# Optimization experiments

Hardware: AMD Instinct MI355X
Metric: run time of the kernel (lower is better)

## Reference

```python
import jax, jax.numpy as jnp
import numpy as np

B, S, D = 16, 1024, 1024  # shape constraints force S == D == 1024


def setup_inputs() -> dict:
    key = jax.random.key(0)
    k1, k2, k3 = jax.random.split(key, 3)
    f1_norm = jax.random.normal(k1, (B, S, D), dtype=jnp.float32)
    f2_norm = jax.random.normal(k2, (B, S, D), dtype=jnp.float32)
    # xavier_normal_ init: std = sqrt(2 / (fan_in + fan_out))
    xavier_std = float(np.sqrt(2.0 / (D + D)))
    corr_weights = jax.random.normal(k3, (D, D), dtype=jnp.float32) * xavier_std
    return {"f1_norm": f1_norm, "f2_norm": f2_norm, "corr_weights": corr_weights}


def reference(f1_norm, f2_norm, corr_weights):
    # a1 = f1 @ W : [B, S, D]
    a1 = jnp.einsum('bsd,de->bse', f1_norm, corr_weights)
    # cc_mat = a1 @ f2^T : [B, S1, S2]
    cc_mat = jnp.einsum('bse,bte->bst', a1, f2_norm)
    audio_att = jax.nn.softmax(cc_mat, axis=1)                      # softmax over S1
    visual_att = jax.nn.softmax(jnp.swapaxes(cc_mat, 1, 2), axis=1)  # [B,S2,S1], softmax over S2
    atten_audiofeatures = jnp.matmul(f1_norm, audio_att)             # [B, S1(=D), S2]
    atten_visualfeatures = jnp.matmul(f2_norm, visual_att)           # [B, S2(=D), S1]
    return (jnp.swapaxes(atten_audiofeatures, 1, 2),
            jnp.swapaxes(atten_visualfeatures, 1, 2))
```

## Files before the change

### kernel.cpp

```cpp
#include <hip/hip_runtime.h>
#include <hip/hip_bf16.h>
#include <stdint.h>

typedef __bf16 bf16_t;
typedef bf16_t bf16x8 __attribute__((ext_vector_type(8)));
typedef bf16_t bf16x4 __attribute__((ext_vector_type(4)));
typedef float  f32x4  __attribute__((ext_vector_type(4)));

#define B_  16
#define S_  1024
#define D_  1024
#define BS_ (B_ * S_)
#define MAT_ (S_ * D_)

#define BAR()   __builtin_amdgcn_s_barrier()
#define LGKM0() asm volatile("s_waitcnt lgkmcnt(0)" ::: "memory")
#define VMC4()  asm volatile("s_waitcnt vmcnt(4)" ::: "memory")

__device__ __forceinline__ void async_load16(const void* g, void* l) {
    __builtin_amdgcn_global_load_lds((__attribute__((address_space(1))) void*)(g),
                                     (__attribute__((address_space(3))) void*)(l),
                                     16, 0, 0);
}

template <int SPLIT, int OSP, int XS, int STATS>
__global__ __launch_bounds__(512, 2)
void gemm8p(const bf16_t* __restrict__ gAh, const bf16_t* __restrict__ gAl,
            const bf16_t* __restrict__ gBh, const bf16_t* __restrict__ gBl,
            float* __restrict__ Cf, bf16_t* __restrict__ Ch, bf16_t* __restrict__ Cl,
            float* __restrict__ Mp2, float* __restrict__ Zp2,
            float* __restrict__ Np2, float* __restrict__ Yp2,
            int M, int N, int K, long sA, long sB, long sC)
{
    (void)M;
    constexpr int BK  = SPLIT ? 32 : 64;
    constexpr int BUF = 65536;
    __shared__ __attribute__((aligned(16))) char smem[2 * BUF];

    const int tid  = threadIdx.x;
    const int w    = tid >> 6;
    const int lane = tid & 63;
    const int wm   = w >> 2;
    const int wn   = w & 3;
    const int fm   = lane & 15;
    const int quad = lane >> 4;

    int bm, bn, b;
    if constexpr (XS == 1) {
        const int flat = (int)blockIdx.x + ((int)blockIdx.y << 2) + ((int)blockIdx.z << 4);
        const int xcd = flat & 7, slot = flat >> 3;
        b  = (xcd << 1) | (slot >> 4);
        bm = (slot >> 2) & 3;
        bn = slot & 3;
    } else if constexpr (XS == 2) {
        const int flat = (int)blockIdx.x + ((int)blockIdx.y << 2) + ((int)blockIdx.z << 4);
        const int xcd = flat & 7, slot = flat >> 3;
        b  = (xcd << 2) | (slot >> 4);
        bm = (slot >> 2) & 3;
        bn = slot & 3;
    } else if constexpr (XS == 3) {
        const int flat = (int)blockIdx.x + ((int)blockIdx.y << 2);
        const int xcd = flat & 7, slot = flat >> 3;
        b  = 0;
        bm = (xcd << 3) | (slot >> 2);
        bn = slot & 3;
    } else {
        bn = blockIdx.x; bm = blockIdx.y; b = blockIdx.z;
    }

    const bf16_t* pAh = gAh; const bf16_t* pAl = gAl;
    const bf16_t* pBh = gBh; const bf16_t* pBl = gBl;
    float* Cfp = Cf;
    if constexpr (XS == 2) {
        if (b >= 16) { pAh = gAl; pBh = gBl; Cfp = Cf + (long)B_ * MAT_; b -= 16; }
    }

    const int NT    = K / BK;
    const int abase = (int)((long)b * sA) + bm * 256 * K;
    const int bbase = (int)((long)b * sB) + bn * 256 * K;

    int aof[2][2], bof[2][2], lof[2][2];
    if constexpr (!SPLIT) {
#pragma unroll
        for (int h = 0; h < 2; ++h)
#pragma unroll
            for (int i = 0; i < 2; ++i) {
                const int o   = h * 16384 + i * 8192 + tid * 16;
                const int row = o >> 7;
                const int c   = ((o >> 4) & 7) ^ (row & 7);
                aof[h][i] = abase + row * K + c * 8;
                bof[h][i] = bbase + row * K + c * 8;
                lof[h][i] = o;
            }
    } else {
#pragma unroll
        for (int h = 0; h < 2; ++h) {
            const int o   = h * 8192 + tid * 16;
            const int row = o >> 6;
            const int c   = ((o >> 4) & 3) ^ ((row >> 1) & 3);
            aof[h][0] = abase + row * K + c * 8;
            bof[h][0] = bbase + row * K + c * 8;
            lof[h][0] = o;
        }
    }

    f32x4 acc[8][4] = {};

    if constexpr (!SPLIT) {
        auto stgA = [&](int t, int h, int lb) {
            const int k = (t < NT ? t : NT - 1) * BK;
            async_load16(pAh + (aof[h][0] + k), smem + lb + lof[h][0]);
            async_load16(pAh + (aof[h][1] + k), smem + lb + lof[h][1]);
        };
        auto stgB = [&](int t, int h, int lb) {
            const int k = (t < NT ? t : NT - 1) * BK;
            async_load16(pBh + (bof[h][0] + k), smem + lb + 32768 + lof[h][0]);
            async_load16(pBh + (bof[h][1] + k), smem + lb + 32768 + lof[h][1]);
        };
        const int xb = (fm & 7) << 4;
        auto ldA = [&](int lb, int m, int ks) -> bf16x8 {
            const int row = wm * 128 + m * 16 + fm;
            return *(const bf16x8*)(smem + lb + row * 128 + ((ks * 64 + quad * 16) ^ xb));
        };
        auto ldB = [&](int lb, int n, int ks) -> bf16x8 {
            const int row = wn * 64 + n * 16 + fm;
            return *(const bf16x8*)(smem + lb + 32768 + row * 128 + ((ks * 64 + quad * 16) ^ xb));
        };

        bf16x8 ar[4][2], br[4][2];
        auto qp = [&](int mh, int nh) {
#pragma unroll
            for (int m = 0; m < 4; ++m)
#pragma unroll
                for (int n = 0; n < 2; ++n) {
                    f32x4 c = acc[mh * 4 + m][nh * 2 + n];
                    c = __builtin_amdgcn_mfma_f32_16x16x32_bf16(ar[m][0], br[nh * 2 + n][0], c, 0, 0, 0);
                    c = __builtin_amdgcn_mfma_f32_16x16x32_bf16(ar[m][1], br[nh * 2 + n][1], c, 0, 0, 0);
                    acc[mh * 4 + m][nh * 2 + n] = c;
                }
        };

        stgA(0, 0, 0); stgA(0, 1, 0); stgB(0, 0, 0); stgB(0, 1, 0);
        stgB(1, 0, BUF); stgB(1, 1, BUF);
        VMC4(); BAR();

        const int NIT = NT >> 1;
        for (int it = 0; it < NIT; ++it) {
            const int t = it << 1;
#pragma unroll
            for (int ph = 0; ph < 2; ++ph) {
                const int rb = ph ? BUF : 0;
                const int ob = ph ? 0 : BUF;
                const int tt = t + ph;
#pragma unroll
                for (int m = 0; m < 4; ++m) { ar[m][0] = ldA(rb, m, 0); ar[m][1] = ldA(rb, m, 1); }
#pragma unroll
                for (int n = 0; n < 2; ++n) { br[n][0] = ldB(rb, n, 0); br[n][1] = ldB(rb, n, 1); }
                stgA(tt + 1, 0, ob);
                BAR(); LGKM0(); __builtin_amdgcn_s_setprio(1);
                qp(0, 0);
                __builtin_amdgcn_s_setprio(0); BAR();
#pragma unroll
                for (int n = 2; n < 4; ++n) { br[n][0] = ldB(rb, n, 0); br[n][1] = ldB(rb, n, 1); }
                stgA(tt + 1, 1, ob);
                BAR(); LGKM0(); __builtin_amdgcn_s_setprio(1);
                qp(0, 1);
                __builtin_amdgcn_s_setprio(0); BAR();
#pragma unroll
                for (int m = 0; m < 4; ++m) { ar[m][0] = ldA(rb, m + 4, 0); ar[m][1] = ldA(rb, m + 4, 1); }
                stgB(tt + 2, 0, rb);
                BAR(); LGKM0(); __builtin_amdgcn_s_setprio(1);
                qp(1, 0);
                __builtin_amdgcn_s_setprio(0); BAR();
                stgB(tt + 2, 1, rb);
                BAR(); LGKM0(); __builtin_amdgcn_s_setprio(1);
                qp(1, 1);
                __builtin_amdgcn_s_setprio(0); VMC4(); BAR();
            }
        }
    } else {
        auto stgAh = [&](int t, int lb) {
            const int k = (t < NT ? t : NT - 1) * BK;
            async_load16(pAh + (aof[0][0] + k), smem + lb + lof[0][0]);
            async_load16(pAh + (aof[1][0] + k), smem + lb + lof[1][0]);
        };
        auto stgAl = [&](int t, int lb) {
            const int k = (t < NT ? t : NT - 1) * BK;
            async_load16(pAl + (aof[0][0] + k), smem + lb + 16384 + lof[0][0]);
            async_load16(pAl + (aof[1][0] + k), smem + lb + 16384 + lof[1][0]);
        };
        auto stgBh = [&](int t, int lb) {
            const int k = (t < NT ? t : NT - 1) * BK;
            async_load16(pBh + (bof[0][0] + k), smem + lb + 32768 + lof[0][0]);
            async_load16(pBh + (bof[1][0] + k), smem + lb + 32768 + lof[1][0]);
        };
        auto stgBl = [&](int t, int lb) {
            const int k = (t < NT ? t : NT - 1) * BK;
            async_load16(pBl + (bof[0][0] + k), smem + lb + 49152 + lof[0][0]);
            async_load16(pBl + (bof[1][0] + k), smem + lb + 49152 + lof[1][0]);
        };
        const int xs2 = ((fm >> 1) & 3) << 4;
        auto ldSA = [&](int lb, int comp, int m) -> bf16x8 {
            const int row = wm * 128 + m * 16 + fm;
            return *(const bf16x8*)(smem + lb + comp * 16384 + row * 64 + ((quad * 16) ^ xs2));
        };
        auto ldSB = [&](int lb, int comp, int n) -> bf16x8 {
            const int row = wn * 64 + n * 16 + fm;
            return *(const bf16x8*)(smem + lb + comp * 16384 + row * 64 + ((quad * 16) ^ xs2));
        };

        bf16x8 arh[4], arl[4], brh[4], brl[4];
        auto qs = [&](int mh, int nh) {
#pragma unroll
            for (int m = 0; m < 4; ++m)
#pragma unroll
                for (int n = 0; n < 2; ++n) {
                    f32x4 c = acc[mh * 4 + m][nh * 2 + n];
                    c = __builtin_amdgcn_mfma_f32_16x16x32_bf16(arh[m], brh[nh * 2 + n], c, 0, 0, 0);
                    c = __builtin_amdgcn_mfma_f32_16x16x32_bf16(arl[m], brh[nh * 2 + n], c, 0, 0, 0);
                    c = __builtin_amdgcn_mfma_f32_16x16x32_bf16(arh[m], brl[nh * 2 + n], c, 0, 0, 0);
                    acc[mh * 4 + m][nh * 2 + n] = c;
                }
        };

        stgAh(0, 0); stgAl(0, 0); stgBh(0, 0); stgBl(0, 0);
        stgBh(1, BUF); stgBl(1, BUF);
        VMC4(); BAR();

        const int NIT = NT >> 1;
        for (int it = 0; it < NIT; ++it) {
            const int t = it << 1;
#pragma unroll
            for (int ph = 0; ph < 2; ++ph) {
                const int rb = ph ? BUF : 0;
                const int ob = ph ? 0 : BUF;
                const int tt = t + ph;
#pragma unroll
                for (int m = 0; m < 4; ++m) { arh[m] = ldSA(rb, 0, m); arl[m] = ldSA(rb, 1, m); }
#pragma unroll
                for (int n = 0; n < 2; ++n) { brh[n] = ldSB(rb, 2, n); brl[n] = ldSB(rb, 3, n); }
                stgAh(tt + 1, ob);
                BAR(); LGKM0(); __builtin_amdgcn_s_setprio(1);
                qs(0, 0);
                __builtin_amdgcn_s_setprio(0); BAR();
#pragma unroll
                for (int n = 2; n < 4; ++n) { brh[n] = ldSB(rb, 2, n); brl[n] = ldSB(rb, 3, n); }
                stgAl(tt + 1, ob);
                BAR(); LGKM0(); __builtin_amdgcn_s_setprio(1);
                qs(0, 1);
                __builtin_amdgcn_s_setprio(0); BAR();
#pragma unroll
                for (int m = 0; m < 4; ++m) { arh[m] = ldSA(rb, 0, m + 4); arl[m] = ldSA(rb, 1, m + 4); }
                stgBh(tt + 2, rb);
                BAR(); LGKM0(); __builtin_amdgcn_s_setprio(1);
                qs(1, 0);
                __builtin_amdgcn_s_setprio(0); BAR();
                stgBl(tt + 2, rb);
                BAR(); LGKM0(); __builtin_amdgcn_s_setprio(1);
                qs(1, 1);
                __builtin_amdgcn_s_setprio(0); VMC4(); BAR();
            }
        }
    }

    float2* colp = (float2*)smem;
    float2* rowp = (float2*)(smem + 4096);
    if constexpr (STATS) {
#pragma unroll
        for (int j = 0; j < 4; ++j) {
            float m = acc[0][j][0];
#pragma unroll
            for (int i = 0; i < 8; ++i)
#pragma unroll
                for (int r = 0; r < 4; ++r) m = fmaxf(m, acc[i][j][r]);
            float z = 0.f;
#pragma unroll
            for (int i = 0; i < 8; ++i)
#pragma unroll
                for (int r = 0; r < 4; ++r) z += __expf(acc[i][j][r] - m);
#pragma unroll
            for (int off = 16; off <= 32; off <<= 1) {
                float mo = __shfl_xor(m, off), zo = __shfl_xor(z, off);
                float nm = fmaxf(m, mo);
                z = z * __expf(m - nm) + zo * __expf(mo - nm); m = nm;
            }
            if (quad == 0) colp[wm * 256 + wn * 64 + j * 16 + fm] = make_float2(m, z);
        }
#pragma unroll
        for (int i = 0; i < 8; ++i)
#pragma unroll
            for (int r = 0; r < 4; ++r) {
                float m = fmaxf(fmaxf(acc[i][0][r], acc[i][1][r]),
                                fmaxf(acc[i][2][r], acc[i][3][r]));
                float z = __expf(acc[i][0][r] - m) + __expf(acc[i][1][r] - m)
                        + __expf(acc[i][2][r] - m) + __expf(acc[i][3][r] - m);
#pragma unroll
                for (int off = 1; off <= 8; off <<= 1) {
                    float mo = __shfl_xor(m, off), zo = __shfl_xor(z, off);
                    float nm = fmaxf(m, mo);
                    z = z * __expf(m - nm) + zo * __expf(mo - nm); m = nm;
                }
                if (fm == 0)
                    rowp[wn * 256 + wm * 128 + i * 16 + quad * 4 + r] = make_float2(m, z);
            }
    }

#pragma unroll
    for (int i = 0; i < 8; ++i) {
        const int row0 = bm * 256 + wm * 128 + i * 16 + quad * 4;
#pragma unroll
        for (int j = 0; j < 4; ++j) {
            const int col = bn * 256 + wn * 64 + j * 16 + fm;
#pragma unroll
            for (int r = 0; r < 4; ++r) {
                const long idx = (long)b * sC + (long)(row0 + r) * N + col;
                const float v = acc[i][j][r];
                if constexpr (OSP) {
                    const bf16_t h = (bf16_t)v;
                    Ch[idx] = h;
                    Cl[idx] = (bf16_t)(v - (float)h);
                } else {
                    Cfp[idx] = v;
                }
            }
        }
    }

    if constexpr (STATS) {
        __syncthreads();
        if (tid < 256) {
            float2 p0 = colp[tid], p1 = colp[256 + tid];
            float nm = fmaxf(p0.x, p1.x);
            float z = p0.y * __expf(p0.x - nm) + p1.y * __expf(p1.x - nm);
            const int gcol = bn * 256 + tid;
            Mp2[((b * 4 + bm) << 10) + gcol] = nm;
            Zp2[((b * 4 + bm) << 10) + gcol] = z;
        } else {
            const int rr = tid - 256;
            float2 p = rowp[rr];
            float m = p.x, z = p.y;
#pragma unroll
            for (int c = 1; c < 4; ++c) {
                float2 q = rowp[c * 256 + rr];
                float nm = fmaxf(m, q.x);
                z = z * __expf(m - nm) + q.y * __expf(q.x - nm); m = nm;
            }
            const int grow = bm * 256 + rr;
            Np2[((b * 4 + bn) << 10) + grow] = m;
            Yp2[((b * 4 + bn) << 10) + grow] = z;
        }
    }
}

__global__ void split2_f32(const float* __restrict__ f1, const float* __restrict__ f2,
                           bf16_t* __restrict__ h1, bf16_t* __restrict__ l1,
                           bf16_t* __restrict__ h2, bf16_t* __restrict__ l2)
{
    const long tot = (long)B_ * MAT_;
    long i = ((long)blockIdx.x * 256 + threadIdx.x) * 4;
    const float* s; bf16_t* h; bf16_t* l;
    if (i < tot) { s = f1; h = h1; l = l1; }
    else { i -= tot; s = f2; h = h2; l = l2; }
    float4 v = *(const float4*)(s + i);
    float a[4] = {v.x, v.y, v.z, v.w};
    bf16x4 hh, ll;
#pragma unroll
    for (int e = 0; e < 4; ++e) {
        const bf16_t hv = (bf16_t)a[e];
        hh[e] = hv;
        ll[e] = (bf16_t)(a[e] - (float)hv);
    }
    *(bf16x4*)(h + i) = hh;
    *(bf16x4*)(l + i) = ll;
}

__global__ void transpose_split_w(const float* __restrict__ W,
                                  bf16_t* __restrict__ Wth, bf16_t* __restrict__ Wtl)
{
    __shared__ float tile[32][33];
    const int d0 = blockIdx.x * 32, e0 = blockIdx.y * 32;
    const int tx = threadIdx.x, ty = threadIdx.y;
    for (int r = ty; r < 32; r += 8)
        tile[r][tx] = W[(long)(d0 + r) * D_ + e0 + tx];
    __syncthreads();
    for (int r = ty; r < 32; r += 8) {
        const float v = tile[tx][r];
        const bf16_t h = (bf16_t)v;
        Wth[(long)(e0 + r) * D_ + d0 + tx] = h;
        Wtl[(long)(e0 + r) * D_ + d0 + tx] = (bf16_t)(v - (float)h);
    }
}

__global__ void combine_stats(const float* __restrict__ Mp2, const float* __restrict__ Zp2,
                              const float* __restrict__ Np2, const float* __restrict__ Yp2,
                              float* __restrict__ Mst, float* __restrict__ Zst,
                              float* __restrict__ Nst, float* __restrict__ Yst)
{
    const int i = blockIdx.x * 256 + threadIdx.x;
    const int which = i >> 14;
    const int idx = i & 16383;
    const int b = idx >> 10, x = idx & 1023;
    const float* P = which ? Np2 : Mp2;
    const float* Q = which ? Yp2 : Zp2;
    const int base = (b << 12) + x;
    float m = P[base], z = Q[base];
#pragma unroll
    for (int c = 1; c < 4; ++c) {
        float mc = P[base + (c << 10)], zc = Q[base + (c << 10)];
        float nm = fmaxf(m, mc);
        z = z * __expf(m - nm) + zc * __expf(mc - nm); m = nm;
    }
    if (which) { Nst[idx] = m; Yst[idx] = z; }
    else       { Mst[idx] = m; Zst[idx] = z; }
}

__global__ void build_atts(const float* __restrict__ cc,
                           const float* __restrict__ Mst, const float* __restrict__ Zst,
                           const float* __restrict__ Nst, const float* __restrict__ Yst,
                           bf16_t* __restrict__ attA, bf16_t* __restrict__ attV)
{
    __shared__ float tile[32][33];
    const int b = blockIdx.z;
    const int s0 = blockIdx.x * 32, t0 = blockIdx.y * 32;
    const int tx = threadIdx.x, ty = threadIdx.y;
    const float* src = cc + (long)b * MAT_;
    bf16_t* dV = attV + (long)b * MAT_;
    bf16_t* dA = attA + (long)b * MAT_;
    for (int r = ty; r < 32; r += 8) {
        const int s = s0 + r;
        const float v = src[(long)s * S_ + t0 + tx];
        tile[r][tx] = v;
        dV[(long)s * S_ + t0 + tx] =
            (bf16_t)(__expf(v - Nst[b * 1024 + s]) * (1.f / Yst[b * 1024 + s]));
    }
    __syncthreads();
    for (int r = ty; r < 32; r += 8) {
        const int t = t0 + r;
        const float m  = Mst[b * 1024 + t];
        const float rz = 1.f / Zst[b * 1024 + t];
        dA[(long)t * S_ + s0 + tx] = (bf16_t)(__expf(tile[tx][r] - m) * rz);
    }
}

extern "C" void kernel_launch(void* const* d_in, const int* in_sizes, int n_in,
                              void* d_out, int out_size, void* d_ws, size_t ws_size,
                              hipStream_t stream)
{
    const float* f1 = (const float*)d_in[0];
    const float* f2 = (const float*)d_in[1];
    const float* W  = (const float*)d_in[2];

    float* out0 = (float*)d_out;
    float* out1 = out0 + (long)B_ * MAT_;

    bf16_t* a1h = (bf16_t*)out0;
    bf16_t* a1l = a1h + (long)B_ * MAT_;
    bf16_t* Wth = (bf16_t*)out1;
    bf16_t* Wtl = Wth + (long)MAT_;
    float*  cc  = out1;

    char* w = (char*)d_ws;
    bf16_t* f1h  = (bf16_t*)(w);
    bf16_t* f2h  = (bf16_t*)(w + (32l << 20));
    bf16_t* f1l  = (bf16_t*)(w + (64l << 20));
    bf16_t* f2l  = (bf16_t*)(w + (96l << 20));
    bf16_t* attA = f1l;
    bf16_t* attV = f2l;
    float*  Mp2  = (float*)(w + (128l << 20));
    float*  Zp2  = Mp2 + 16 * 4 * 1024;
    float*  Np2  = Zp2 + 16 * 4 * 1024;
    float*  Yp2  = Np2 + 16 * 4 * 1024;
    float*  Mst  = Yp2 + 16 * 4 * 1024;
    float*  Zst  = Mst + BS_;
    float*  Nst  = Zst + BS_;
    float*  Yst  = Nst + BS_;

    split2_f32<<<32768, 256, 0, stream>>>(f1, f2, f1h, f1l, f2h, f2l);
    transpose_split_w<<<dim3(32, 32), dim3(32, 8), 0, stream>>>(W, Wth, Wtl);

    gemm8p<1, 1, 3, 0><<<dim3(4, 64, 1), 512, 0, stream>>>(
        f1h, f1l, Wth, Wtl, nullptr, a1h, a1l,
        nullptr, nullptr, nullptr, nullptr, BS_, 1024, 1024, 0, 0, 0);

    gemm8p<1, 0, 1, 1><<<dim3(4, 4, 16), 512, 0, stream>>>(
        a1h, a1l, f2h, f2l, cc, nullptr, nullptr,
        Mp2, Zp2, Np2, Yp2, 1024, 1024, 1024, MAT_, MAT_, MAT_);

    combine_stats<<<128, 256, 0, stream>>>(Mp2, Zp2, Np2, Yp2, Mst, Zst, Nst, Yst);

    build_atts<<<dim3(32, 32, 16), dim3(32, 8), 0, stream>>>(
        cc, Mst, Zst, Nst, Yst, attA, attV);

    gemm8p<0, 0, 2, 0><<<dim3(4, 4, 32), 512, 0, stream>>>(
        attA, attV, f1h, f2h, out0, nullptr, nullptr,
        nullptr, nullptr, nullptr, nullptr, 1024, 1024, 1024, MAT_, MAT_, MAT_);
}
```

Baseline: 504.8 us.

## Fuse split kernels, fold stats combine into build_atts, restructure final GEMM

Merges the f1/f2 split and W transpose-split into one launch, and folds the partial softmax-stat combination into build_atts so the combine_stats kernel and the Mst/Zst buffers go away. The final attention GEMM now runs both outputs sequentially in each block over half the grid, with its own epilogue. The GEMM pipelines also reorder async stage issues ahead of LDS reads and replace explicit lgkmcnt waits with sched_barrier. Together these cut launch overhead and extra memory passes, but halving the final GEMM grid lowers parallelism, and dropping the explicit LDS waits relies on the compiler inserting correct waits.

```diff
diff --git a/kernel.cpp b/kernel.cpp
--- a/kernel.cpp
+++ b/kernel.cpp
@@ -14,8 +14,10 @@
 #define MAT_ (S_ * D_)
 
 #define BAR()   __builtin_amdgcn_s_barrier()
-#define LGKM0() asm volatile("s_waitcnt lgkmcnt(0)" ::: "memory")
 #define VMC4()  asm volatile("s_waitcnt vmcnt(4)" ::: "memory")
+#define SBAR0() __builtin_amdgcn_sched_barrier(0)
+#define PRIO1() __builtin_amdgcn_s_setprio(1)
+#define PRIO0() __builtin_amdgcn_s_setprio(0)
 
 __device__ __forceinline__ void async_load16(const void* g, void* l) {
     __builtin_amdgcn_global_load_lds((__attribute__((address_space(1))) void*)(g),
@@ -46,16 +48,10 @@
     const int quad = lane >> 4;
 
     int bm, bn, b;
-    if constexpr (XS == 1) {
+    if constexpr (XS == 1 || XS == 2) {
         const int flat = (int)blockIdx.x + ((int)blockIdx.y << 2) + ((int)blockIdx.z << 4);
         const int xcd = flat & 7, slot = flat >> 3;
         b  = (xcd << 1) | (slot >> 4);
-        bm = (slot >> 2) & 3;
-        bn = slot & 3;
-    } else if constexpr (XS == 2) {
-        const int flat = (int)blockIdx.x + ((int)blockIdx.y << 2) + ((int)blockIdx.z << 4);
-        const int xcd = flat & 7, slot = flat >> 3;
-        b  = (xcd << 2) | (slot >> 4);
         bm = (slot >> 2) & 3;
         bn = slot & 3;
     } else if constexpr (XS == 3) {
@@ -68,13 +64,6 @@
         bn = blockIdx.x; bm = blockIdx.y; b = blockIdx.z;
     }
 
-    const bf16_t* pAh = gAh; const bf16_t* pAl = gAl;
-    const bf16_t* pBh = gBh; const bf16_t* pBl = gBl;
-    float* Cfp = Cf;
-    if constexpr (XS == 2) {
-        if (b >= 16) { pAh = gAl; pBh = gBl; Cfp = Cf + (long)B_ * MAT_; b -= 16; }
-    }
-
     const int NT    = K / BK;
     const int abase = (int)((long)b * sA) + bm * 256 * K;
     const int bbase = (int)((long)b * sB) + bn * 256 * K;
@@ -107,15 +96,19 @@
     f32x4 acc[8][4] = {};
 
     if constexpr (!SPLIT) {
+        constexpr int NHALF = (XS == 2) ? 2 : 1;
+        const bf16_t* pA = gAh;
+        const bf16_t* pB = gBh;
+
         auto stgA = [&](int t, int h, int lb) {
             const int k = (t < NT ? t : NT - 1) * BK;
-            async_load16(pAh + (aof[h][0] + k), smem + lb + lof[h][0]);
-            async_load16(pAh + (aof[h][1] + k), smem + lb + lof[h][1]);
+            async_load16(pA + (aof[h][0] + k), smem + lb + lof[h][0]);
+            async_load16(pA + (aof[h][1] + k), smem + lb + lof[h][1]);
         };
         auto stgB = [&](int t, int h, int lb) {
             const int k = (t < NT ? t : NT - 1) * BK;
-            async_load16(pBh + (bof[h][0] + k), smem + lb + 32768 + lof[h][0]);
-            async_load16(pBh + (bof[h][1] + k), smem + lb + 32768 + lof[h][1]);
+            async_load16(pB + (bof[h][0] + k), smem + lb + 32768 + lof[h][0]);
+            async_load16(pB + (bof[h][1] + k), smem + lb + 32768 + lof[h][1]);
         };
         const int xb = (fm & 7) << 4;
         auto ldA = [&](int lb, int m, int ks) -> bf16x8 {
@@ -140,64 +133,89 @@
                 }
         };
 
-        stgA(0, 0, 0); stgA(0, 1, 0); stgB(0, 0, 0); stgB(0, 1, 0);
-        stgB(1, 0, BUF); stgB(1, 1, BUF);
-        VMC4(); BAR();
-
-        const int NIT = NT >> 1;
-        for (int it = 0; it < NIT; ++it) {
-            const int t = it << 1;
-#pragma unroll
-            for (int ph = 0; ph < 2; ++ph) {
-                const int rb = ph ? BUF : 0;
-                const int ob = ph ? 0 : BUF;
-                const int tt = t + ph;
-#pragma unroll
-                for (int m = 0; m < 4; ++m) { ar[m][0] = ldA(rb, m, 0); ar[m][1] = ldA(rb, m, 1); }
-#pragma unroll
-                for (int n = 0; n < 2; ++n) { br[n][0] = ldB(rb, n, 0); br[n][1] = ldB(rb, n, 1); }
-                stgA(tt + 1, 0, ob);
-                BAR(); LGKM0(); __builtin_amdgcn_s_setprio(1);
-                qp(0, 0);
-                __builtin_amdgcn_s_setprio(0); BAR();
-#pragma unroll
-                for (int n = 2; n < 4; ++n) { br[n][0] = ldB(rb, n, 0); br[n][1] = ldB(rb, n, 1); }
-                stgA(tt + 1, 1, ob);
-                BAR(); LGKM0(); __builtin_amdgcn_s_setprio(1);
-                qp(0, 1);
-                __builtin_amdgcn_s_setprio(0); BAR();
-#pragma unroll
-                for (int m = 0; m < 4; ++m) { ar[m][0] = ldA(rb, m + 4, 0); ar[m][1] = ldA(rb, m + 4, 1); }
-                stgB(tt + 2, 0, rb);
-                BAR(); LGKM0(); __builtin_amdgcn_s_setprio(1);
-                qp(1, 0);
-                __builtin_amdgcn_s_setprio(0); BAR();
-                stgB(tt + 2, 1, rb);
-                BAR(); LGKM0(); __builtin_amdgcn_s_setprio(1);
-                qp(1, 1);
-                __builtin_amdgcn_s_setprio(0); VMC4(); BAR();
-            }
-        }
+        for (int half = 0; half < NHALF; ++half) {
+            if constexpr (XS == 2) {
+                pA = half ? gAl : gAh;
+                pB = half ? gBl : gBh;
+            }
+            float* Cfp = Cf + (half ? (long)B_ * MAT_ : 0);
+#pragma unroll
+            for (int i = 0; i < 8; ++i)
+#pragma unroll
+                for (int j = 0; j < 4; ++j) acc[i][j] = f32x4{0.f, 0.f, 0.f, 0.f};
+
+            stgA(0, 0, 0); stgA(0, 1, 0); stgB(0, 0, 0); stgB(0, 1, 0);
+            stgB(1, 0, BUF); stgB(1, 1, BUF);
+            VMC4(); BAR();
+
+            const int NIT = NT >> 1;
+            for (int it = 0; it < NIT; ++it) {
+                const int t = it << 1;
+#pragma unroll
+                for (int ph = 0; ph < 2; ++ph) {
+                    const int rb = ph ? BUF : 0;
+                    const int ob = ph ? 0 : BUF;
+                    const int tt = t + ph;
+                    stgA(tt + 1, 0, ob);
+#pragma unroll
+                    for (int m = 0; m < 4; ++m) { ar[m][0] = ldA(rb, m, 0); ar[m][1] = ldA(rb, m, 1); }
+#pragma unroll
+                    for (int n = 0; n < 2; ++n) { br[n][0] = ldB(rb, n, 0); br[n][1] = ldB(rb, n, 1); }
+                    BAR(); PRIO1();
+                    qp(0, 0);
+                    PRIO0(); SBAR0(); BAR();
+                    stgA(tt + 1, 1, ob);
+#pragma unroll
+                    for (int n = 2; n < 4; ++n) { br[n][0] = ldB(rb, n, 0); br[n][1] = ldB(rb, n, 1); }
+                    BAR(); PRIO1();
+                    qp(0, 1);
+                    PRIO0(); SBAR0(); BAR();
+                    stgB(tt + 2, 0, rb);
+#pragma unroll
+                    for (int m = 0; m < 4; ++m) { ar[m][0] = ldA(rb, m + 4, 0); ar[m][1] = ldA(rb, m + 4, 1); }
+                    BAR(); PRIO1();
+                    qp(1, 0);
+                    PRIO0(); SBAR0(); BAR();
+                    stgB(tt + 2, 1, rb);
+                    BAR(); PRIO1();
+                    qp(1, 1);
+                    PRIO0(); SBAR0(); VMC4(); BAR();
+                }
+            }
+
+#pragma unroll
+            for (int i = 0; i < 8; ++i) {
+                const int row0 = bm * 256 + wm * 128 + i * 16 + quad * 4;
+#pragma unroll
+                for (int j = 0; j < 4; ++j) {
+                    const int col = bn * 256 + wn * 64 + j * 16 + fm;
+#pragma unroll
+                    for (int r = 0; r < 4; ++r)
+                        Cfp[(long)b * sC + (long)(row0 + r) * N + col] = acc[i][j][r];
+                }
+            }
+        }
+        return;
     } else {
         auto stgAh = [&](int t, int lb) {
             const int k = (t < NT ? t : NT - 1) * BK;
-            async_load16(pAh + (aof[0][0] + k), smem + lb + lof[0][0]);
-            async_load16(pAh + (aof[1][0] + k), smem + lb + lof[1][0]);
+            async_load16(gAh + (aof[0][0] + k), smem + lb + lof[0][0]);
+            async_load16(gAh + (aof[1][0] + k), smem + lb + lof[1][0]);
         };
         auto stgAl = [&](int t, int lb) {
             const int k = (t < NT ? t : NT - 1) * BK;
-            async_load16(pAl + (aof[0][0] + k), smem + lb + 16384 + lof[0][0]);
-            async_load16(pAl + (aof[1][0] + k), smem + lb + 16384 + lof[1][0]);
+            async_load16(gAl + (aof[0][0] + k), smem + lb + 16384 + lof[0][0]);
+            async_load16(gAl + (aof[1][0] + k), smem + lb + 16384 + lof[1][0]);
         };
         auto stgBh = [&](int t, int lb) {
             const int k = (t < NT ? t : NT - 1) * BK;
-            async_load16(pBh + (bof[0][0] + k), smem + lb + 32768 + lof[0][0]);
-            async_load16(pBh + (bof[1][0] + k), smem + lb + 32768 + lof[1][0]);
+            async_load16(gBh + (bof[0][0] + k), smem + lb + 32768 + lof[0][0]);
+            async_load16(gBh + (bof[1][0] + k), smem + lb + 32768 + lof[1][0]);
         };
         auto stgBl = [&](int t, int lb) {
             const int k = (t < NT ? t : NT - 1) * BK;
-            async_load16(pBl + (bof[0][0] + k), smem + lb + 49152 + lof[0][0]);
-            async_load16(pBl + (bof[1][0] + k), smem + lb + 49152 + lof[1][0]);
+            async_load16(gBl + (bof[0][0] + k), smem + lb + 49152 + lof[0][0]);
+            async_load16(gBl + (bof[1][0] + k), smem + lb + 49152 + lof[1][0]);
         };
         const int xs2 = ((fm >> 1) & 3) << 4;
         auto ldSA = [&](int lb, int comp, int m) -> bf16x8 {
@@ -235,30 +253,30 @@
                 const int rb = ph ? BUF : 0;
                 const int ob = ph ? 0 : BUF;
                 const int tt = t + ph;
+                stgAh(tt + 1, ob);
 #pragma unroll
                 for (int m = 0; m < 4; ++m) { arh[m] = ldSA(rb, 0, m); arl[m] = ldSA(rb, 1, m); }
 #pragma unroll
                 for (int n = 0; n < 2; ++n) { brh[n] = ldSB(rb, 2, n); brl[n] = ldSB(rb, 3, n); }
-                stgAh(tt + 1, ob);
-                BAR(); LGKM0(); __builtin_amdgcn_s_setprio(1);
+                BAR(); PRIO1();
                 qs(0, 0);
-                __builtin_amdgcn_s_setprio(0); BAR();
+                PRIO0(); SBAR0(); BAR();
+                stgAl(tt + 1, ob);
 #pragma unroll
                 for (int n = 2; n < 4; ++n) { brh[n] = ldSB(rb, 2, n); brl[n] = ldSB(rb, 3, n); }
-                stgAl(tt + 1, ob);
-                BAR(); LGKM0(); __builtin_amdgcn_s_setprio(1);
+                BAR(); PRIO1();
                 qs(0, 1);
-                __builtin_amdgcn_s_setprio(0); BAR();
+                PRIO0(); SBAR0(); BAR();
+                stgBh(tt + 2, rb);
 #pragma unroll
                 for (int m = 0; m < 4; ++m) { arh[m] = ldSA(rb, 0, m + 4); arl[m] = ldSA(rb, 1, m + 4); }
-                stgBh(tt + 2, rb);
-                BAR(); LGKM0(); __builtin_amdgcn_s_setprio(1);
+                BAR(); PRIO1();
                 qs(1, 0);
-                __builtin_amdgcn_s_setprio(0); BAR();
+                PRIO0(); SBAR0(); BAR();
                 stgBl(tt + 2, rb);
-                BAR(); LGKM0(); __builtin_amdgcn_s_setprio(1);
+                BAR(); PRIO1();
                 qs(1, 1);
-                __builtin_amdgcn_s_setprio(0); VMC4(); BAR();
+                PRIO0(); SBAR0(); VMC4(); BAR();
             }
         }
     }
@@ -320,7 +338,7 @@
                     Ch[idx] = h;
                     Cl[idx] = (bf16_t)(v - (float)h);
                 } else {
-                    Cfp[idx] = v;
+                    Cf[idx] = v;
                 }
             }
         }
@@ -352,77 +370,85 @@
     }
 }
 
-__global__ void split2_f32(const float* __restrict__ f1, const float* __restrict__ f2,
-                           bf16_t* __restrict__ h1, bf16_t* __restrict__ l1,
-                           bf16_t* __restrict__ h2, bf16_t* __restrict__ l2)
-{
-    const long tot = (long)B_ * MAT_;
-    long i = ((long)blockIdx.x * 256 + threadIdx.x) * 4;
-    const float* s; bf16_t* h; bf16_t* l;
-    if (i < tot) { s = f1; h = h1; l = l1; }
-    else { i -= tot; s = f2; h = h2; l = l2; }
-    float4 v = *(const float4*)(s + i);
-    float a[4] = {v.x, v.y, v.z, v.w};
-    bf16x4 hh, ll;
-#pragma unroll
-    for (int e = 0; e < 4; ++e) {
-        const bf16_t hv = (bf16_t)a[e];
-        hh[e] = hv;
-        ll[e] = (bf16_t)(a[e] - (float)hv);
-    }
-    *(bf16x4*)(h + i) = hh;
-    *(bf16x4*)(l + i) = ll;
-}
-
-__global__ void transpose_split_w(const float* __restrict__ W,
-                                  bf16_t* __restrict__ Wth, bf16_t* __restrict__ Wtl)
+__global__ void split_all(const float* __restrict__ f1, const float* __restrict__ f2,
+                          const float* __restrict__ W,
+                          bf16_t* __restrict__ h1, bf16_t* __restrict__ l1,
+                          bf16_t* __restrict__ h2, bf16_t* __restrict__ l2,
+                          bf16_t* __restrict__ Wth, bf16_t* __restrict__ Wtl)
 {
     __shared__ float tile[32][33];
-    const int d0 = blockIdx.x * 32, e0 = blockIdx.y * 32;
-    const int tx = threadIdx.x, ty = threadIdx.y;
-    for (int r = ty; r < 32; r += 8)
-        tile[r][tx] = W[(long)(d0 + r) * D_ + e0 + tx];
-    __syncthreads();
-    for (int r = ty; r < 32; r += 8) {
-        const float v = tile[tx][r];
-        const bf16_t h = (bf16_t)v;
-        Wth[(long)(e0 + r) * D_ + d0 + tx] = h;
-        Wtl[(long)(e0 + r) * D_ + d0 + tx] = (bf16_t)(v - (float)h);
+    const int bid = blockIdx.x;
+    if (bid < 32768) {
+        const long tot = (long)B_ * MAT_;
+        long i = ((long)bid * 256 + threadIdx.x) * 4;
+        const float* s; bf16_t* h; bf16_t* l;
+        if (i < tot) { s = f1; h = h1; l = l1; }
+        else { i -= tot; s = f2; h = h2; l = l2; }
+        float4 v = *(const float4*)(s + i);
+        float a[4] = {v.x, v.y, v.z, v.w};
+        bf16x4 hh, ll;
+#pragma unroll
+        for (int e = 0; e < 4; ++e) {
+            const bf16_t hv = (bf16_t)a[e];
+            hh[e] = hv;
+            ll[e] = (bf16_t)(a[e] - (float)hv);
+        }
+        *(bf16x4*)(h + i) = hh;
+        *(bf16x4*)(l + i) = ll;
+    } else {
+        const int b2 = bid - 32768;
+        const int d0 = (b2 & 31) * 32, e0 = (b2 >> 5) * 32;
+        const int tx = threadIdx.x & 31, ty = threadIdx.x >> 5;
+        for (int r = ty; r < 32; r += 8)
+            tile[r][tx] = W[(long)(d0 + r) * D_ + e0 + tx];
+        __syncthreads();
+        for (int r = ty; r < 32; r += 8) {
+            const float v = tile[tx][r];
+            const bf16_t h = (bf16_t)v;
+            Wth[(long)(e0 + r) * D_ + d0 + tx] = h;
+            Wtl[(long)(e0 + r) * D_ + d0 + tx] = (bf16_t)(v - (float)h);
+        }
     }
 }
 
-__global__ void combine_stats(const float* __restrict__ Mp2, const float* __restrict__ Zp2,
-                              const float* __restrict__ Np2, const float* __restrict__ Yp2,
-                              float* __restrict__ Mst, float* __restrict__ Zst,
-                              float* __restrict__ Nst, float* __restrict__ Yst)
-{
-    const int i = blockIdx.x * 256 + threadIdx.x;
-    const int which = i >> 14;
-    const int idx = i & 16383;
-    const int b = idx >> 10, x = idx & 1023;
-    const float* P = which ? Np2 : Mp2;
-    const float* Q = which ? Yp2 : Zp2;
-    const int base = (b << 12) + x;
-    float m = P[base], z = Q[base];
-#pragma unroll
-    for (int c = 1; c < 4; ++c) {
-        float mc = P[base + (c << 10)], zc = Q[base + (c << 10)];
-        float nm = fmaxf(m, mc);
-        z = z * __expf(m - nm) + zc * __expf(mc - nm); m = nm;
-    }
-    if (which) { Nst[idx] = m; Yst[idx] = z; }
-    else       { Mst[idx] = m; Zst[idx] = z; }
-}
-
 __global__ void build_atts(const float* __restrict__ cc,
-                           const float* __restrict__ Mst, const float* __restrict__ Zst,
-                           const float* __restrict__ Nst, const float* __restrict__ Yst,
+                           const float* __restrict__ Mp2, const float* __restrict__ Zp2,
+                           const float* __restrict__ Np2, const float* __restrict__ Yp2,
                            bf16_t* __restrict__ attA, bf16_t* __restrict__ attV)
 {
     __shared__ float tile[32][33];
+    __shared__ float tm[32], tz[32], sm[32], sz[32];
     const int b = blockIdx.z;
     const int s0 = blockIdx.x * 32, t0 = blockIdx.y * 32;
     const int tx = threadIdx.x, ty = threadIdx.y;
+    const int flat = ty * 32 + tx;
+
+    if (flat < 32) {
+        const int t = t0 + flat;
+        float m = Mp2[((b * 4) << 10) + t], z = Zp2[((b * 4) << 10) + t];
+#pragma unroll
+        for (int c = 1; c < 4; ++c) {
+            float mc = Mp2[((b * 4 + c) << 10) + t];
+            float zc = Zp2[((b * 4 + c) << 10) + t];
+            float nm = fmaxf(m, mc);
+            z = z * __expf(m - nm) + zc * __expf(mc - nm); m = nm;
+        }
+        tm[flat] = m; tz[flat] = 1.f / z;
+    } else if (flat < 64) {
+        const int ii = flat - 32;
+        const int s = s0 + ii;
+        float m = Np2[((b * 4) << 10) + s], z = Yp2[((b * 4) << 10) + s];
+#pragma unroll
+        for (int c = 1; c < 4; ++c) {
+            float mc = Np2[((b * 4 + c) << 10) + s];
+            float zc = Yp2[((b * 4 + c) << 10) + s];
+            float nm = fmaxf(m, mc);
+            z = z * __expf(m - nm) + zc * __expf(mc - nm); m = nm;
+        }
+        sm[ii] = m; sz[ii] = 1.f / z;
+    }
+    __syncthreads();
+
     const float* src = cc + (long)b * MAT_;
     bf16_t* dV = attV + (long)b * MAT_;
     bf16_t* dA = attA + (long)b * MAT_;
@@ -430,15 +456,12 @@
         const int s = s0 + r;
         const float v = src[(long)s * S_ + t0 + tx];
         tile[r][tx] = v;
-        dV[(long)s * S_ + t0 + tx] =
-            (bf16_t)(__expf(v - Nst[b * 1024 + s]) * (1.f / Yst[b * 1024 + s]));
+        dV[(long)s * S_ + t0 + tx] = (bf16_t)(__expf(v - sm[r]) * sz[r]);
     }
     __syncthreads();
     for (int r = ty; r < 32; r += 8) {
         const int t = t0 + r;
-        const float m  = Mst[b * 1024 + t];
-        const float rz = 1.f / Zst[b * 1024 + t];
-        dA[(long)t * S_ + s0 + tx] = (bf16_t)(__expf(tile[tx][r] - m) * rz);
+        dA[(long)t * S_ + s0 + tx] = (bf16_t)(__expf(tile[tx][r] - tm[r]) * tz[r]);
     }
 }
 
@@ -470,13 +493,8 @@
     float*  Zp2  = Mp2 + 16 * 4 * 1024;
     float*  Np2  = Zp2 + 16 * 4 * 1024;
     float*  Yp2  = Np2 + 16 * 4 * 1024;
-    float*  Mst  = Yp2 + 16 * 4 * 1024;
-    float*  Zst  = Mst + BS_;
-    float*  Nst  = Zst + BS_;
-    float*  Yst  = Nst + BS_;
-
-    split2_f32<<<32768, 256, 0, stream>>>(f1, f2, f1h, f1l, f2h, f2l);
-    transpose_split_w<<<dim3(32, 32), dim3(32, 8), 0, stream>>>(W, Wth, Wtl);
+
+    split_all<<<33792, 256, 0, stream>>>(f1, f2, W, f1h, f1l, f2h, f2l, Wth, Wtl);
 
     gemm8p<1, 1, 3, 0><<<dim3(4, 64, 1), 512, 0, stream>>>(
         f1h, f1l, Wth, Wtl, nullptr, a1h, a1l,
@@ -486,12 +504,10 @@
         a1h, a1l, f2h, f2l, cc, nullptr, nullptr,
         Mp2, Zp2, Np2, Yp2, 1024, 1024, 1024, MAT_, MAT_, MAT_);
 
-    combine_stats<<<128, 256, 0, stream>>>(Mp2, Zp2, Np2, Yp2, Mst, Zst, Nst, Yst);
-
     build_atts<<<dim3(32, 32, 16), dim3(32, 8), 0, stream>>>(
-        cc, Mst, Zst, Nst, Yst, attA, attV);
-
-    gemm8p<0, 0, 2, 0><<<dim3(4, 4, 32), 512, 0, stream>>>(
+        cc, Mp2, Zp2, Np2, Yp2, attA, attV);
+
+    gemm8p<0, 0, 2, 0><<<dim3(4, 4, 16), 512, 0, stream>>>(
         attA, attV, f1h, f2h, out0, nullptr, nullptr,
         nullptr, nullptr, nullptr, nullptr, 1024, 1024, 1024, MAT_, MAT_, MAT_);
 }
```

New measurement: 533.1 us. 5.6% more time.
